# Performance work log

Hardware: AMD Instinct MI355X
Metric: run time of the kernel (lower is better)

## Reference

```python
import jax, jax.numpy as jnp
import numpy as np

K_SIZE = 5  # kernel_size=[5]


def setup_inputs() -> dict:
    key = jax.random.key(0)
    k1, k2 = jax.random.split(key)
    bs, N, h, w, c = 4, 8, 256, 256, 1
    frames = jax.random.normal(k1, (bs, N, h, w, c), dtype=jnp.float32)
    core = jax.random.normal(k2, (bs, h, w, N * K_SIZE * K_SIZE * c), dtype=jnp.float32)
    return {"frames": frames, "core": core}


def _kpn_filter(frames, core):
    # frames: (bs, N, h, w, c); core: (bs, h, w, N*K*K*c)
    bs, N, h, w, c = frames.shape
    K = K_SIZE
    # _convert_dict: raw reshape of core to (bs, N, h, w, c, K*K)
    core_r = jnp.reshape(core, (bs, N, h, w, c, K * K))
    p = K // 2
    fpad = jnp.pad(frames, ((0, 0), (0, 0), (p, p), (p, p), (0, 0)))
    # K*K shifted views stacked on last axis: (bs, N, h, w, c, K*K)
    img_stack = jnp.stack(
        [fpad[:, :, i:i + h, j:j + w, :] for i in range(K) for j in range(K)],
        axis=-1,
    )
    # per-pixel dynamic-kernel weighted sum
    pred_img_i = jnp.sum(core_r * img_stack, axis=-1)  # (bs, N, h, w, c)
    # single kernel size -> mean over kernel axis is identity
    pred_img = jnp.mean(pred_img_i, axis=1)  # (bs, h, w, c), mean over burst N
    return pred_img, pred_img_i


def reference(frames, core):
    return _kpn_filter(frames, core)
```

## Files before the change

kernel.cpp:

```cpp
#include <hip/hip_runtime.h>

#define H 256
#define W 256
#define NB 8
#define BS 4

__global__ __launch_bounds__(256, 3)
void kpn_main(const float* __restrict__ frames, const float* __restrict__ core,
              float* __restrict__ pred_i) {
  __shared__ float lds[8][264];

  const int tid = threadIdx.x;
  const int blk = blockIdx.x;
  const int g   = blk * 256 + tid;
  const int bn  = g >> 14;
  const int y0  = (blk & 63) * 4;

  const float4* c4 = (const float4*)(core + (size_t)g * 100);
  float ws[100];
#pragma unroll
  for (int k = 0; k < 25; ++k) {
    float4 t = c4[k];
    ws[4 * k + 0] = t.x; ws[4 * k + 1] = t.y;
    ws[4 * k + 2] = t.z; ws[4 * k + 3] = t.w;
  }

  const float* fbase = frames + (size_t)bn * (H * W);
  {
    const int r  = tid >> 5;
    const int c  = tid & 31;
    const int yy = y0 + r - 2;
    float4 z  = make_float4(0.f, 0.f, 0.f, 0.f);
    float4 v0 = z, v1 = z;
    if ((unsigned)yy < (unsigned)H) {
      const float4* src = (const float4*)(fbase + (size_t)yy * W + c * 8);
      v0 = src[0]; v1 = src[1];
    }
    float* dst = &lds[r][c * 8 + 4];
    *(float4*)(dst)     = v0;
    *(float4*)(dst + 4) = v1;
    if (c == 0)  *(float4*)(&lds[r][0])   = z;
    if (c == 31) *(float4*)(&lds[r][260]) = z;
  }
  __syncthreads();

  const int x0 = (tid & 63) * 4;
  const int yl = tid >> 6;
  float acc[4] = {0.f, 0.f, 0.f, 0.f};
#pragma unroll
  for (int ki = 0; ki < 5; ++ki) {
    const float4* lrow = (const float4*)&lds[yl + ki][x0];
    float4 a0 = lrow[0], a1 = lrow[1], a2 = lrow[2];
    float fr[12] = {a0.x, a0.y, a0.z, a0.w,
                    a1.x, a1.y, a1.z, a1.w,
                    a2.x, a2.y, a2.z, a2.w};
#pragma unroll
    for (int kj = 0; kj < 5; ++kj) {
      const int kidx = ki * 5 + kj;
#pragma unroll
      for (int p = 0; p < 4; ++p) {
        acc[p] += ws[p * 25 + kidx] * fr[p + kj + 2];
      }
    }
  }
  *(float4*)(pred_i + (size_t)g * 4) = make_float4(acc[0], acc[1], acc[2], acc[3]);
}

__global__ __launch_bounds__(256)
void kpn_mean(const float* __restrict__ pred_i, float* __restrict__ pred) {
  int g = blockIdx.x * 256 + threadIdx.x;
  int b  = g >> 14;
  int yx = g & 16383;
  const float4* src = (const float4*)pred_i + (size_t)b * (NB * 16384) + yx;
  float4 s = make_float4(0.f, 0.f, 0.f, 0.f);
#pragma unroll
  for (int n = 0; n < NB; ++n) {
    float4 v = src[(size_t)n * 16384];
    s.x += v.x; s.y += v.y; s.z += v.z; s.w += v.w;
  }
  s.x *= 0.125f; s.y *= 0.125f; s.z *= 0.125f; s.w *= 0.125f;
  ((float4*)pred)[g] = s;
}

extern "C" void kernel_launch(void* const* d_in, const int* in_sizes, int n_in,
                              void* d_out, int out_size, void* d_ws, size_t ws_size,
                              hipStream_t stream) {
  const float* frames = (const float*)d_in[0];
  const float* core   = (const float*)d_in[1];
  float* pred   = (float*)d_out;
  float* pred_i = pred + (size_t)BS * H * W;

  hipLaunchKernelGGL(kpn_main, dim3(2048), dim3(256), 0, stream,
                     frames, core, pred_i);
  hipLaunchKernelGGL(kpn_mean, dim3(256), dim3(256), 0, stream,
                     pred_i, pred);
}
```

Before: 42.70 us.

## Fuse burst-mean into main KPN kernel by remapping blocks across burst frames

Blocks are remapped so each one covers all 8 burst frames for a half-row of one output row. The burst mean can then be reduced in shared memory and written directly, removing the second kernel launch and its re-read of pred_i. Core loads and output stores switch to nontemporal hints. The cost is a larger shared-memory tile with less halo reuse across rows (5 rows per output row instead of 8 per 4), an extra synchronisation, and a reduction done by only 32 threads.

```diff
diff --git a/kernel.cpp b/kernel.cpp
--- a/kernel.cpp
+++ b/kernel.cpp
@@ -2,84 +2,80 @@
 
 #define H 256
 #define W 256
-#define NB 8
-#define BS 4
+
+typedef float f4 __attribute__((ext_vector_type(4)));
 
 __global__ __launch_bounds__(256, 3)
-void kpn_main(const float* __restrict__ frames, const float* __restrict__ core,
-              float* __restrict__ pred_i) {
-  __shared__ float lds[8][264];
+void kpn_fused(const float* __restrict__ frames, const float* __restrict__ core,
+               float* __restrict__ pred, float* __restrict__ pred_i) {
+  __shared__ f4 smem[8 * 5 * 34];
 
   const int tid = threadIdx.x;
   const int blk = blockIdx.x;
-  const int g   = blk * 256 + tid;
-  const int bn  = g >> 14;
-  const int y0  = (blk & 63) * 4;
+  const int xh  = blk & 1;
+  const int y   = (blk >> 1) & 255;
+  const int b   = blk >> 9;
 
-  const float4* c4 = (const float4*)(core + (size_t)g * 100);
+  const int n = tid >> 5;
+  const int q = tid & 31;
+
+  const int g = ((b * 8 + n) * 256 + y) * 64 + xh * 32 + q;
+  const f4* c4 = (const f4*)(core + (size_t)g * 100);
   float ws[100];
 #pragma unroll
   for (int k = 0; k < 25; ++k) {
-    float4 t = c4[k];
-    ws[4 * k + 0] = t.x; ws[4 * k + 1] = t.y;
-    ws[4 * k + 2] = t.z; ws[4 * k + 3] = t.w;
+    f4 t = __builtin_nontemporal_load(c4 + k);
+    ws[4 * k + 0] = t[0]; ws[4 * k + 1] = t[1];
+    ws[4 * k + 2] = t[2]; ws[4 * k + 3] = t[3];
   }
 
-  const float* fbase = frames + (size_t)bn * (H * W);
-  {
-    const int r  = tid >> 5;
-    const int c  = tid & 31;
-    const int yy = y0 + r - 2;
-    float4 z  = make_float4(0.f, 0.f, 0.f, 0.f);
-    float4 v0 = z, v1 = z;
-    if ((unsigned)yy < (unsigned)H) {
-      const float4* src = (const float4*)(fbase + (size_t)yy * W + c * 8);
-      v0 = src[0]; v1 = src[1];
+  for (int i = tid; i < 8 * 5 * 34; i += 256) {
+    const int nn  = i / 170;
+    const int rem = i - nn * 170;
+    const int r   = rem / 34;
+    const int c   = rem - r * 34;
+    const int yy  = y + r - 2;
+    const int x4  = xh * 128 + (c - 1) * 4;
+    f4 v = {0.f, 0.f, 0.f, 0.f};
+    if ((unsigned)yy < (unsigned)H && (unsigned)x4 <= 252u) {
+      v = *(const f4*)(frames + ((size_t)(b * 8 + nn) * H + yy) * W + x4);
     }
-    float* dst = &lds[r][c * 8 + 4];
-    *(float4*)(dst)     = v0;
-    *(float4*)(dst + 4) = v1;
-    if (c == 0)  *(float4*)(&lds[r][0])   = z;
-    if (c == 31) *(float4*)(&lds[r][260]) = z;
+    smem[i] = v;
   }
   __syncthreads();
 
-  const int x0 = (tid & 63) * 4;
-  const int yl = tid >> 6;
-  float acc[4] = {0.f, 0.f, 0.f, 0.f};
+  f4 acc = {0.f, 0.f, 0.f, 0.f};
 #pragma unroll
   for (int ki = 0; ki < 5; ++ki) {
-    const float4* lrow = (const float4*)&lds[yl + ki][x0];
-    float4 a0 = lrow[0], a1 = lrow[1], a2 = lrow[2];
-    float fr[12] = {a0.x, a0.y, a0.z, a0.w,
-                    a1.x, a1.y, a1.z, a1.w,
-                    a2.x, a2.y, a2.z, a2.w};
+    const f4* row = &smem[(n * 5 + ki) * 34 + q];
+    f4 a0 = row[0], a1 = row[1], a2 = row[2];
+    float fr[12] = {a0[0], a0[1], a0[2], a0[3],
+                    a1[0], a1[1], a1[2], a1[3],
+                    a2[0], a2[1], a2[2], a2[3]};
 #pragma unroll
     for (int kj = 0; kj < 5; ++kj) {
-      const int kidx = ki * 5 + kj;
 #pragma unroll
       for (int p = 0; p < 4; ++p) {
-        acc[p] += ws[p * 25 + kidx] * fr[p + kj + 2];
+        acc[p] += ws[p * 25 + ki * 5 + kj] * fr[p + kj + 2];
       }
     }
   }
-  *(float4*)(pred_i + (size_t)g * 4) = make_float4(acc[0], acc[1], acc[2], acc[3]);
-}
+  __builtin_nontemporal_store(acc, (f4*)(pred_i + (size_t)g * 4));
 
-__global__ __launch_bounds__(256)
-void kpn_mean(const float* __restrict__ pred_i, float* __restrict__ pred) {
-  int g = blockIdx.x * 256 + threadIdx.x;
-  int b  = g >> 14;
-  int yx = g & 16383;
-  const float4* src = (const float4*)pred_i + (size_t)b * (NB * 16384) + yx;
-  float4 s = make_float4(0.f, 0.f, 0.f, 0.f);
+  __syncthreads();
+  f4* red = smem;
+  red[tid] = acc;
+  __syncthreads();
+  if (tid < 32) {
+    f4 s = {0.f, 0.f, 0.f, 0.f};
 #pragma unroll
-  for (int n = 0; n < NB; ++n) {
-    float4 v = src[(size_t)n * 16384];
-    s.x += v.x; s.y += v.y; s.z += v.z; s.w += v.w;
+    for (int k = 0; k < 8; ++k) {
+      s += red[tid + 32 * k];
+    }
+    s *= 0.125f;
+    __builtin_nontemporal_store(
+        s, (f4*)(pred + ((size_t)b * 256 + y) * 256 + xh * 128 + tid * 4));
   }
-  s.x *= 0.125f; s.y *= 0.125f; s.z *= 0.125f; s.w *= 0.125f;
-  ((float4*)pred)[g] = s;
 }
 
 extern "C" void kernel_launch(void* const* d_in, const int* in_sizes, int n_in,
@@ -88,10 +84,8 @@
   const float* frames = (const float*)d_in[0];
   const float* core   = (const float*)d_in[1];
   float* pred   = (float*)d_out;
-  float* pred_i = pred + (size_t)BS * H * W;
+  float* pred_i = pred + (size_t)4 * H * W;
 
-  hipLaunchKernelGGL(kpn_main, dim3(2048), dim3(256), 0, stream,
-                     frames, core, pred_i);
-  hipLaunchKernelGGL(kpn_mean, dim3(256), dim3(256), 0, stream,
-                     pred_i, pred);
+  hipLaunchKernelGGL(kpn_fused, dim3(2048), dim3(256), 0, stream,
+                     frames, core, pred, pred_i);
 }
```

Result: slower. 134.6 us (+215.2%).
